# Performance work log

Measured on AMD Instinct MI355X. Metric: run time of the kernel, lower is better.

## Reference

```python
import jax, jax.numpy as jnp
import numpy as np

NEG_SLOPE = 0.2  # DenseGATConv default negative_slope


def dense_gat(x, adj, W, att_src, att_dst, bias):
    # x: [B,N,Cin], adj: [B,N,N] (self-loops already added), W: [Cin,H*C]
    B, N, _ = x.shape
    H, C = att_src.shape
    h = (x @ W).reshape(B, N, H, C)
    a_src = jnp.einsum('bnhc,hc->bnh', h, att_src)  # [B,N,H]
    a_dst = jnp.einsum('bnhc,hc->bnh', h, att_dst)
    # alpha[b,i,j,h] = a_src[b,j,h] + a_dst[b,i,h]  (softmax over j, axis=2)
    alpha = a_src[:, None, :, :] + a_dst[:, :, None, :]
    alpha = jnp.where(alpha >= 0, alpha, NEG_SLOPE * alpha)  # leaky_relu
    mask = (adj != 0)[..., None]  # [B,N,N,1]
    alpha = jax.nn.softmax(jnp.where(mask, alpha, -1e30), axis=2)
    out = jnp.einsum('bijh,bjhc->bihc', alpha, h).reshape(B, N, H * C)
    return out + bias


def setup_inputs() -> dict:
    key = jax.random.key(0)
    ks = jax.random.split(key, 8)
    B, N, D = 1, 8192, 128
    x = jax.random.normal(ks[0], (B, N, D), dtype=jnp.float32)
    adj = (jax.random.uniform(ks[1], (B, N, N)) < 0.01).astype(jnp.float32)
    idx = jnp.arange(N)
    adj = adj.at[:, idx, idx].set(1.0)  # DenseGATConv add_loop=True
    s = 1.0 / np.sqrt(D)
    lin = lambda k: jax.random.uniform(k, (D, D), minval=-s, maxval=s, dtype=jnp.float32)
    att = lambda k: jax.random.normal(k, (1, D), dtype=jnp.float32) * 0.1  # heads=1
    return dict(
        x=x, adj=adj,
        W0=lin(ks[2]), att_src0=att(ks[3]), att_dst0=att(ks[4]), b0=jnp.zeros((D,), jnp.float32),
        W1=lin(ks[5]), att_src1=att(ks[6]), att_dst1=att(ks[7]), b1=jnp.zeros((D,), jnp.float32),
    )


def reference(x, adj, W0, att_src0, att_dst0, b0, W1, att_src1, att_dst1, b1):
    out0 = dense_gat(x, adj, W0, att_src0, att_dst0, b0)
    out0 = jax.nn.relu(out0)  # relu_layers_index = [0]
    out1 = dense_gat(out0, adj, W1, att_src1, att_dst1, b1)
    # dropout_rate = 0 -> dropout is identity; squeeze batch dim as in block
    return (out0[0], out1[0])
```

## Files before the change

### kernel.cpp

```cpp
#include <hip/hip_runtime.h>

#define MAXDEG 192
#define NEG_SLOPE 0.2f
#define D 128

__device__ __forceinline__ float bf2f(unsigned short u) {
    return __uint_as_float(((unsigned)u) << 16);
}
__device__ __forceinline__ unsigned short f2bf(float f) {
    unsigned u = __float_as_uint(f);
    return (unsigned short)((u + 0x7fffu + ((u >> 16) & 1u)) >> 16);
}
__device__ __forceinline__ int is_f32(const void* adj) {
    return ((const unsigned*)adj)[0] == 0x3F800000u;
}

__global__ __launch_bounds__(256) void build_ell(
        const void* __restrict__ adj,
        unsigned short* __restrict__ cols, int* __restrict__ deg, int N) {
    __shared__ int cnt[4];
    const int w = threadIdx.x >> 6, lane = threadIdx.x & 63;
    const int row = blockIdx.x * 4 + w;
    if (lane == 0) cnt[w] = 0;
    __syncthreads();
    unsigned short* crow = cols + (size_t)row * MAXDEG;
    if (is_f32(adj)) {
        const float4* arow = (const float4*)((const float*)adj + (size_t)row * N);
        const int nv = N / 4;
        for (int v = lane; v < nv; v += 128) {
            float4 u0 = arow[v];
            float4 u1 = arow[v + 64];
            const unsigned* a0 = (const unsigned*)&u0;
            const unsigned* a1 = (const unsigned*)&u1;
            #pragma unroll
            for (int e = 0; e < 4; e++)
                if (a0[e]) { int p = atomicAdd(&cnt[w], 1); if (p < MAXDEG) crow[p] = (unsigned short)(v * 4 + e); }
            #pragma unroll
            for (int e = 0; e < 4; e++)
                if (a1[e]) { int p = atomicAdd(&cnt[w], 1); if (p < MAXDEG) crow[p] = (unsigned short)((v + 64) * 4 + e); }
        }
    } else {
        const uint4* arow = (const uint4*)((const unsigned short*)adj + (size_t)row * N);
        const int nv = N / 8;
        for (int v = lane; v < nv; v += 128) {
            uint4 u0 = arow[v];
            uint4 u1 = arow[v + 64];
            const unsigned short* s0 = (const unsigned short*)&u0;
            const unsigned short* s1 = (const unsigned short*)&u1;
            #pragma unroll
            for (int e = 0; e < 8; e++)
                if (s0[e]) { int p = atomicAdd(&cnt[w], 1); if (p < MAXDEG) crow[p] = (unsigned short)(v * 8 + e); }
            #pragma unroll
            for (int e = 0; e < 8; e++)
                if (s1[e]) { int p = atomicAdd(&cnt[w], 1); if (p < MAXDEG) crow[p] = (unsigned short)((v + 64) * 8 + e); }
        }
    }
    __syncthreads();
    if (lane == 0) deg[row] = cnt[w] < MAXDEG ? cnt[w] : MAXDEG;
}

__global__ __launch_bounds__(256) void gemm128(
        const void* __restrict__ A, const void* __restrict__ W,
        const void* __restrict__ adjFlag, float* __restrict__ H,
        const void* __restrict__ attS, const void* __restrict__ attD,
        float* __restrict__ asrc, float* __restrict__ adst, int a_force_f32) {
    __shared__ float xs[32 * D];
    __shared__ float wsf[64 * D];
    const int tid = threadIdx.x;
    const size_t row0 = (size_t)blockIdx.x * 32;
    const int f32m = is_f32(adjFlag);
    const int aF = a_force_f32 | f32m;

    if (aF) {
        const float4* av = (const float4*)((const float*)A + row0 * D);
        float4* xl = (float4*)xs;
        #pragma unroll
        for (int k = 0; k < 4; k++) xl[tid + 256 * k] = av[tid + 256 * k];
    } else {
        const uint4* av = (const uint4*)((const unsigned short*)A + row0 * D);
        #pragma unroll
        for (int k = 0; k < 2; k++) {
            uint4 u = av[tid + 256 * k];
            const unsigned short* us = (const unsigned short*)&u;
            #pragma unroll
            for (int e = 0; e < 8; e++) xs[(tid + 256 * k) * 8 + e] = bf2f(us[e]);
        }
    }

    const int tx = tid & 31, ty = tid >> 5;
    const int c0 = tx * 4, r0 = ty * 4;
    float acc[4][4] = {};
    for (int p = 0; p < 2; p++) {
        __syncthreads();
        if (f32m) {
            const float4* wv = (const float4*)((const float*)W + (size_t)p * 64 * D);
            float4* wl = (float4*)wsf;
            #pragma unroll
            for (int k = 0; k < 8; k++) wl[tid + 256 * k] = wv[tid + 256 * k];
        } else {
            const uint4* wv = (const uint4*)((const unsigned short*)W + (size_t)p * 64 * D);
            #pragma unroll
            for (int k = 0; k < 4; k++) {
                uint4 u = wv[tid + 256 * k];
                const unsigned short* us = (const unsigned short*)&u;
                #pragma unroll
                for (int e = 0; e < 8; e++) wsf[(tid + 256 * k) * 8 + e] = bf2f(us[e]);
            }
        }
        __syncthreads();
        #pragma unroll 8
        for (int k = 0; k < 64; k++) {
            float4 wv = *(const float4*)&wsf[k * D + c0];
            #pragma unroll
            for (int i = 0; i < 4; i++) {
                float xv = xs[(r0 + i) * D + p * 64 + k];
                acc[i][0] += xv * wv.x; acc[i][1] += xv * wv.y;
                acc[i][2] += xv * wv.z; acc[i][3] += xv * wv.w;
            }
        }
    }
    float* Ho = H + row0 * D;
    #pragma unroll
    for (int i = 0; i < 4; i++)
        *(float4*)&Ho[(r0 + i) * D + c0] =
            make_float4(acc[i][0], acc[i][1], acc[i][2], acc[i][3]);

    float aSv[4], aDv[4];
    #pragma unroll
    for (int j = 0; j < 4; j++) {
        aSv[j] = f32m ? ((const float*)attS)[c0 + j] : bf2f(((const unsigned short*)attS)[c0 + j]);
        aDv[j] = f32m ? ((const float*)attD)[c0 + j] : bf2f(((const unsigned short*)attD)[c0 + j]);
    }
    #pragma unroll
    for (int i = 0; i < 4; i++) {
        float s = acc[i][0] * aSv[0] + acc[i][1] * aSv[1] + acc[i][2] * aSv[2] + acc[i][3] * aSv[3];
        float d = acc[i][0] * aDv[0] + acc[i][1] * aDv[1] + acc[i][2] * aDv[2] + acc[i][3] * aDv[3];
        #pragma unroll
        for (int off = 16; off > 0; off >>= 1) {
            s += __shfl_down(s, off, 32);
            d += __shfl_down(d, off, 32);
        }
        if (tx == 0) {
            asrc[row0 + r0 + i] = s;
            adst[row0 + r0 + i] = d;
        }
    }
}

__global__ __launch_bounds__(256) void aggregate(
        const float* __restrict__ H,
        const float* __restrict__ asrc, const float* __restrict__ adst,
        const unsigned short* __restrict__ cols, const int* __restrict__ deg,
        const void* __restrict__ bias, const void* __restrict__ adjFlag,
        float* __restrict__ outF, void* __restrict__ outAny,
        size_t elemOff, int relu) {
    __shared__ float scn[4][MAXDEG];
    __shared__ unsigned short sjj[4][MAXDEG];
    const int w = threadIdx.x >> 6, lane = threadIdx.x & 63;
    const int i = blockIdx.x * 4 + w;
    const int d = deg[i];
    const float ai = adst[i];
    const unsigned short* crow = cols + (size_t)i * MAXDEG;

    const int s0 = lane, s1 = lane + 64, s2 = lane + 128;
    unsigned short j0 = 0, j1 = 0, j2 = 0;
    float e0 = -3e38f, e1 = -3e38f, e2 = -3e38f;
    if (s0 < d) { j0 = crow[s0]; float e = asrc[j0] + ai; e0 = (e >= 0.f) ? e : NEG_SLOPE * e; }
    if (s1 < d) { j1 = crow[s1]; float e = asrc[j1] + ai; e1 = (e >= 0.f) ? e : NEG_SLOPE * e; }
    if (s2 < d) { j2 = crow[s2]; float e = asrc[j2] + ai; e2 = (e >= 0.f) ? e : NEG_SLOPE * e; }
    float m = fmaxf(e0, fmaxf(e1, e2));
    #pragma unroll
    for (int off = 1; off < 64; off <<= 1) m = fmaxf(m, __shfl_xor(m, off));
    float p0 = (s0 < d) ? __expf(e0 - m) : 0.f;
    float p1 = (s1 < d) ? __expf(e1 - m) : 0.f;
    float p2 = (s2 < d) ? __expf(e2 - m) : 0.f;
    float l = p0 + p1 + p2;
    #pragma unroll
    for (int off = 1; off < 64; off <<= 1) l += __shfl_xor(l, off);
    const float invl = 1.f / l;
    scn[w][s0] = p0 * invl; sjj[w][s0] = j0;
    scn[w][s1] = p1 * invl; sjj[w][s1] = j1;
    scn[w][s2] = p2 * invl; sjj[w][s2] = j2;
    __syncthreads();

    const float2* H2 = (const float2*)H;
    float2 a0 = {0.f, 0.f}, a1 = {0.f, 0.f}, a2 = {0.f, 0.f}, a3 = {0.f, 0.f};
    int k = 0;
    for (; k + 3 < d; k += 4) {
        const int ja = sjj[w][k], jb = sjj[w][k + 1], jc = sjj[w][k + 2], jd = sjj[w][k + 3];
        const float wa = scn[w][k], wb = scn[w][k + 1], wc = scn[w][k + 2], wd = scn[w][k + 3];
        const float2 va = H2[(size_t)ja * 64 + lane];
        const float2 vb = H2[(size_t)jb * 64 + lane];
        const float2 vc = H2[(size_t)jc * 64 + lane];
        const float2 vd = H2[(size_t)jd * 64 + lane];
        a0.x += wa * va.x; a0.y += wa * va.y;
        a1.x += wb * vb.x; a1.y += wb * vb.y;
        a2.x += wc * vc.x; a2.y += wc * vc.y;
        a3.x += wd * vd.x; a3.y += wd * vd.y;
    }
    for (; k < d; k++) {
        const int j = sjj[w][k];
        const float wk = scn[w][k];
        const float2 v = H2[(size_t)j * 64 + lane];
        a0.x += wk * v.x; a0.y += wk * v.y;
    }
    float vx = a0.x + a1.x + a2.x + a3.x;
    float vy = a0.y + a1.y + a2.y + a3.y;

    const int f32m = is_f32(adjFlag);
    const int c0 = lane * 2;
    const float b0 = f32m ? ((const float*)bias)[c0]     : bf2f(((const unsigned short*)bias)[c0]);
    const float b1 = f32m ? ((const float*)bias)[c0 + 1] : bf2f(((const unsigned short*)bias)[c0 + 1]);
    vx += b0; vy += b1;
    if (relu) { vx = fmaxf(vx, 0.f); vy = fmaxf(vy, 0.f); }
    if (outF) ((float2*)outF)[(size_t)i * 64 + lane] = make_float2(vx, vy);
    if (f32m) {
        ((float2*)outAny)[(elemOff >> 1) + (size_t)i * 64 + lane] = make_float2(vx, vy);
    } else {
        unsigned packed = (unsigned)f2bf(vx) | ((unsigned)f2bf(vy) << 16);
        ((unsigned*)outAny)[(elemOff >> 1) + (size_t)i * 64 + lane] = packed;
    }
}

extern "C" void kernel_launch(void* const* d_in, const int* in_sizes, int n_in,
                              void* d_out, int out_size, void* d_ws, size_t ws_size,
                              hipStream_t stream) {
    const int N = in_sizes[0] / D;

    char* w = (char*)d_ws;
    int* deg             = (int*)w;            w += (size_t)N * sizeof(int);
    unsigned short* cols = (unsigned short*)w; w += (size_t)N * MAXDEG * sizeof(unsigned short);
    float* h             = (float*)w;          w += (size_t)N * D * sizeof(float);
    float* out0          = (float*)w;          w += (size_t)N * D * sizeof(float);
    float* asrc          = (float*)w;          w += (size_t)N * sizeof(float);
    float* adst          = (float*)w;

    const void* adj = d_in[1];

    build_ell<<<N / 4, 256, 0, stream>>>(adj, cols, deg, N);

    gemm128<<<N / 32, 256, 0, stream>>>(d_in[0], d_in[2], adj, h,
                                        d_in[3], d_in[4], asrc, adst, 0);
    aggregate<<<N / 4, 256, 0, stream>>>(h, asrc, adst, cols, deg, d_in[5], adj,
                                         out0, d_out, 0, 1);

    gemm128<<<N / 32, 256, 0, stream>>>(out0, d_in[6], adj, h,
                                        d_in[7], d_in[8], asrc, adst, 1);
    aggregate<<<N / 4, 256, 0, stream>>>(h, asrc, adst, cols, deg, d_in[9], adj,
                                         nullptr, d_out, (size_t)N * D, 0);
}
```

Measured before the change: 459.0 us.

## Fuse all GAT stages into one persistent kernel with grid barriers

Replaces the five kernel launches with a single persistent kernel of 1024 blocks that runs layer-0 GEMM, ELL construction, aggregation, layer-1 GEMM and aggregation in sequence, separated by atomic-counter grid barriers. ELL rows are handed out dynamically through an atomic work queue so that GEMM blocks overlap with adjacency scanning. The GEMM weight staging is cut to 32-row chunks so shared memory fits four blocks per CU. The aim is to remove launch gaps and tail effects, at the cost of barrier spin overhead and a deadlock risk if not all 1024 blocks are co-resident.

```diff
diff --git a/kernel.cpp b/kernel.cpp
--- a/kernel.cpp
+++ b/kernel.cpp
@@ -3,6 +3,8 @@
 #define MAXDEG 192
 #define NEG_SLOPE 0.2f
 #define D 128
+#define NBLK 1024
+#define TPB 256
 
 __device__ __forceinline__ float bf2f(unsigned short u) {
     return __uint_as_float(((unsigned)u) << 16);
@@ -15,16 +17,29 @@
     return ((const unsigned*)adj)[0] == 0x3F800000u;
 }
 
-__global__ __launch_bounds__(256) void build_ell(
-        const void* __restrict__ adj,
-        unsigned short* __restrict__ cols, int* __restrict__ deg, int N) {
-    __shared__ int cnt[4];
+__device__ __forceinline__ void grid_sync(int* bar, int target) {
+    __syncthreads();
+    __threadfence();
+    if (threadIdx.x == 0) {
+        atomicAdd(bar, 1);
+        while (__hip_atomic_load(bar, __ATOMIC_RELAXED, __HIP_MEMORY_SCOPE_AGENT) < target)
+            __builtin_amdgcn_s_sleep(2);
+    }
+    __syncthreads();
+    __threadfence();
+}
+
+__device__ __forceinline__ void ell_group(
+        int g, const void* __restrict__ adj, int N, int f32m,
+        unsigned short* __restrict__ cols, int* __restrict__ deg,
+        float* __restrict__ smem) {
+    int* cnt = (int*)smem;
     const int w = threadIdx.x >> 6, lane = threadIdx.x & 63;
-    const int row = blockIdx.x * 4 + w;
+    const int row = g * 4 + w;
     if (lane == 0) cnt[w] = 0;
     __syncthreads();
     unsigned short* crow = cols + (size_t)row * MAXDEG;
-    if (is_f32(adj)) {
+    if (f32m) {
         const float4* arow = (const float4*)((const float*)adj + (size_t)row * N);
         const int nv = N / 4;
         for (int v = lane; v < nv; v += 128) {
@@ -59,17 +74,15 @@
     if (lane == 0) deg[row] = cnt[w] < MAXDEG ? cnt[w] : MAXDEG;
 }
 
-__global__ __launch_bounds__(256) void gemm128(
-        const void* __restrict__ A, const void* __restrict__ W,
-        const void* __restrict__ adjFlag, float* __restrict__ H,
-        const void* __restrict__ attS, const void* __restrict__ attD,
-        float* __restrict__ asrc, float* __restrict__ adst, int a_force_f32) {
-    __shared__ float xs[32 * D];
-    __shared__ float wsf[64 * D];
+__device__ __forceinline__ void gemm_tile(
+        int t, const void* __restrict__ A, const void* __restrict__ W,
+        int aF, int f32m, const void* __restrict__ attS, const void* __restrict__ attD,
+        float* __restrict__ H, float* __restrict__ asrc, float* __restrict__ adst,
+        float* __restrict__ smem) {
+    float* xs = smem;
+    float* ws = smem + 4096;
     const int tid = threadIdx.x;
-    const size_t row0 = (size_t)blockIdx.x * 32;
-    const int f32m = is_f32(adjFlag);
-    const int aF = a_force_f32 | f32m;
+    const size_t row0 = (size_t)t * 32;
 
     if (aF) {
         const float4* av = (const float4*)((const float*)A + row0 * D);
@@ -90,30 +103,30 @@
     const int tx = tid & 31, ty = tid >> 5;
     const int c0 = tx * 4, r0 = ty * 4;
     float acc[4][4] = {};
-    for (int p = 0; p < 2; p++) {
+    for (int p = 0; p < 4; p++) {
         __syncthreads();
         if (f32m) {
-            const float4* wv = (const float4*)((const float*)W + (size_t)p * 64 * D);
-            float4* wl = (float4*)wsf;
-            #pragma unroll
-            for (int k = 0; k < 8; k++) wl[tid + 256 * k] = wv[tid + 256 * k];
+            const float4* wv = (const float4*)((const float*)W + (size_t)p * 32 * D);
+            float4* wl = (float4*)ws;
+            #pragma unroll
+            for (int k = 0; k < 4; k++) wl[tid + 256 * k] = wv[tid + 256 * k];
         } else {
-            const uint4* wv = (const uint4*)((const unsigned short*)W + (size_t)p * 64 * D);
-            #pragma unroll
-            for (int k = 0; k < 4; k++) {
+            const uint4* wv = (const uint4*)((const unsigned short*)W + (size_t)p * 32 * D);
+            #pragma unroll
+            for (int k = 0; k < 2; k++) {
                 uint4 u = wv[tid + 256 * k];
                 const unsigned short* us = (const unsigned short*)&u;
                 #pragma unroll
-                for (int e = 0; e < 8; e++) wsf[(tid + 256 * k) * 8 + e] = bf2f(us[e]);
+                for (int e = 0; e < 8; e++) ws[(tid + 256 * k) * 8 + e] = bf2f(us[e]);
             }
         }
         __syncthreads();
         #pragma unroll 8
-        for (int k = 0; k < 64; k++) {
-            float4 wv = *(const float4*)&wsf[k * D + c0];
+        for (int k = 0; k < 32; k++) {
+            float4 wv = *(const float4*)&ws[k * D + c0];
             #pragma unroll
             for (int i = 0; i < 4; i++) {
-                float xv = xs[(r0 + i) * D + p * 64 + k];
+                float xv = xs[(r0 + i) * D + p * 32 + k];
                 acc[i][0] += xv * wv.x; acc[i][1] += xv * wv.y;
                 acc[i][2] += xv * wv.z; acc[i][3] += xv * wv.w;
             }
@@ -147,20 +160,19 @@
     }
 }
 
-__global__ __launch_bounds__(256) void aggregate(
-        const float* __restrict__ H,
+__device__ __forceinline__ void agg_row(
+        int row, const float* __restrict__ H,
         const float* __restrict__ asrc, const float* __restrict__ adst,
         const unsigned short* __restrict__ cols, const int* __restrict__ deg,
-        const void* __restrict__ bias, const void* __restrict__ adjFlag,
+        const void* __restrict__ bias, int f32m,
         float* __restrict__ outF, void* __restrict__ outAny,
-        size_t elemOff, int relu) {
-    __shared__ float scn[4][MAXDEG];
-    __shared__ unsigned short sjj[4][MAXDEG];
+        size_t off2, int relu, float* __restrict__ smem) {
     const int w = threadIdx.x >> 6, lane = threadIdx.x & 63;
-    const int i = blockIdx.x * 4 + w;
-    const int d = deg[i];
-    const float ai = adst[i];
-    const unsigned short* crow = cols + (size_t)i * MAXDEG;
+    float* scn = smem + w * MAXDEG;
+    unsigned short* sjj = (unsigned short*)(smem + 4 * MAXDEG) + w * MAXDEG;
+    const int d = deg[row];
+    const float ai = adst[row];
+    const unsigned short* crow = cols + (size_t)row * MAXDEG;
 
     const int s0 = lane, s1 = lane + 64, s2 = lane + 128;
     unsigned short j0 = 0, j1 = 0, j2 = 0;
@@ -178,17 +190,16 @@
     #pragma unroll
     for (int off = 1; off < 64; off <<= 1) l += __shfl_xor(l, off);
     const float invl = 1.f / l;
-    scn[w][s0] = p0 * invl; sjj[w][s0] = j0;
-    scn[w][s1] = p1 * invl; sjj[w][s1] = j1;
-    scn[w][s2] = p2 * invl; sjj[w][s2] = j2;
-    __syncthreads();
+    scn[s0] = p0 * invl; sjj[s0] = j0;
+    scn[s1] = p1 * invl; sjj[s1] = j1;
+    scn[s2] = p2 * invl; sjj[s2] = j2;
 
     const float2* H2 = (const float2*)H;
-    float2 a0 = {0.f, 0.f}, a1 = {0.f, 0.f}, a2 = {0.f, 0.f}, a3 = {0.f, 0.f};
+    float2 a0 = make_float2(0.f, 0.f), a1 = a0, a2 = a0, a3 = a0;
     int k = 0;
     for (; k + 3 < d; k += 4) {
-        const int ja = sjj[w][k], jb = sjj[w][k + 1], jc = sjj[w][k + 2], jd = sjj[w][k + 3];
-        const float wa = scn[w][k], wb = scn[w][k + 1], wc = scn[w][k + 2], wd = scn[w][k + 3];
+        const int ja = sjj[k], jb = sjj[k + 1], jc = sjj[k + 2], jd = sjj[k + 3];
+        const float wa = scn[k], wb = scn[k + 1], wc = scn[k + 2], wd = scn[k + 3];
         const float2 va = H2[(size_t)ja * 64 + lane];
         const float2 vb = H2[(size_t)jb * 64 + lane];
         const float2 vc = H2[(size_t)jc * 64 + lane];
@@ -199,26 +210,75 @@
         a3.x += wd * vd.x; a3.y += wd * vd.y;
     }
     for (; k < d; k++) {
-        const int j = sjj[w][k];
-        const float wk = scn[w][k];
+        const int j = sjj[k];
+        const float wk = scn[k];
         const float2 v = H2[(size_t)j * 64 + lane];
         a0.x += wk * v.x; a0.y += wk * v.y;
     }
     float vx = a0.x + a1.x + a2.x + a3.x;
     float vy = a0.y + a1.y + a2.y + a3.y;
 
-    const int f32m = is_f32(adjFlag);
     const int c0 = lane * 2;
-    const float b0 = f32m ? ((const float*)bias)[c0]     : bf2f(((const unsigned short*)bias)[c0]);
-    const float b1 = f32m ? ((const float*)bias)[c0 + 1] : bf2f(((const unsigned short*)bias)[c0 + 1]);
-    vx += b0; vy += b1;
+    const float bx = f32m ? ((const float*)bias)[c0]     : bf2f(((const unsigned short*)bias)[c0]);
+    const float by = f32m ? ((const float*)bias)[c0 + 1] : bf2f(((const unsigned short*)bias)[c0 + 1]);
+    vx += bx; vy += by;
     if (relu) { vx = fmaxf(vx, 0.f); vy = fmaxf(vy, 0.f); }
-    if (outF) ((float2*)outF)[(size_t)i * 64 + lane] = make_float2(vx, vy);
+    if (outF) ((float2*)outF)[(size_t)row * 64 + lane] = make_float2(vx, vy);
     if (f32m) {
-        ((float2*)outAny)[(elemOff >> 1) + (size_t)i * 64 + lane] = make_float2(vx, vy);
+        ((float2*)outAny)[off2 + (size_t)row * 64 + lane] = make_float2(vx, vy);
     } else {
         unsigned packed = (unsigned)f2bf(vx) | ((unsigned)f2bf(vy) << 16);
-        ((unsigned*)outAny)[(elemOff >> 1) + (size_t)i * 64 + lane] = packed;
+        ((unsigned*)outAny)[off2 + (size_t)row * 64 + lane] = packed;
+    }
+}
+
+__global__ __launch_bounds__(TPB, 4) void gat_mega(
+        const void* __restrict__ x, const void* __restrict__ adj,
+        const void* __restrict__ W0, const void* __restrict__ aS0,
+        const void* __restrict__ aD0, const void* __restrict__ b0,
+        const void* __restrict__ W1, const void* __restrict__ aS1,
+        const void* __restrict__ aD1, const void* __restrict__ b1,
+        void* __restrict__ out, int N,
+        int* __restrict__ bar, int* __restrict__ qhead,
+        int* __restrict__ deg, unsigned short* __restrict__ cols,
+        float* __restrict__ h, float* __restrict__ out0,
+        float* __restrict__ asrc, float* __restrict__ adst) {
+    __shared__ float smem[8192];
+    __shared__ int sgrp;
+    const int bid = blockIdx.x, tid = threadIdx.x;
+    const int f32m = is_f32(adj);
+    const int GT = N / 32;
+    const int NG = N / 4;
+
+    if (bid < GT)
+        gemm_tile(bid, x, W0, f32m, f32m, aS0, aD0, h, asrc, adst, smem);
+    __syncthreads();
+    for (;;) {
+        if (tid == 0) sgrp = atomicAdd(qhead, 1);
+        __syncthreads();
+        const int g = sgrp;
+        __syncthreads();
+        if (g >= NG) break;
+        ell_group(g, adj, N, f32m, cols, deg, smem);
+    }
+    grid_sync(bar, NBLK);
+
+    {
+        const int gw = bid * 4 + (tid >> 6);
+        for (int r = gw; r < N; r += NBLK * 4)
+            agg_row(r, h, asrc, adst, cols, deg, b0, f32m, out0, out, 0, 1, smem);
+    }
+    grid_sync(bar, 2 * NBLK);
+
+    if (bid < GT)
+        gemm_tile(bid, out0, W1, 1, f32m, aS1, aD1, h, asrc, adst, smem);
+    grid_sync(bar, 3 * NBLK);
+
+    {
+        const int gw = bid * 4 + (tid >> 6);
+        for (int r = gw; r < N; r += NBLK * 4)
+            agg_row(r, h, asrc, adst, cols, deg, b1, f32m, nullptr, out,
+                    (size_t)N * (D / 2), 0, smem);
     }
 }
 
@@ -228,6 +288,9 @@
     const int N = in_sizes[0] / D;
 
     char* w = (char*)d_ws;
+    int* bar             = (int*)w;
+    int* qhead           = (int*)(w + 64);
+    w += 256;
     int* deg             = (int*)w;            w += (size_t)N * sizeof(int);
     unsigned short* cols = (unsigned short*)w; w += (size_t)N * MAXDEG * sizeof(unsigned short);
     float* h             = (float*)w;          w += (size_t)N * D * sizeof(float);
@@ -235,17 +298,10 @@
     float* asrc          = (float*)w;          w += (size_t)N * sizeof(float);
     float* adst          = (float*)w;
 
-    const void* adj = d_in[1];
-
-    build_ell<<<N / 4, 256, 0, stream>>>(adj, cols, deg, N);
-
-    gemm128<<<N / 32, 256, 0, stream>>>(d_in[0], d_in[2], adj, h,
-                                        d_in[3], d_in[4], asrc, adst, 0);
-    aggregate<<<N / 4, 256, 0, stream>>>(h, asrc, adst, cols, deg, d_in[5], adj,
-                                         out0, d_out, 0, 1);
-
-    gemm128<<<N / 32, 256, 0, stream>>>(out0, d_in[6], adj, h,
-                                        d_in[7], d_in[8], asrc, adst, 1);
-    aggregate<<<N / 4, 256, 0, stream>>>(h, asrc, adst, cols, deg, d_in[9], adj,
-                                         nullptr, d_out, (size_t)N * D, 0);
-}
+    hipMemsetAsync(d_ws, 0, 256, stream);
+
+    gat_mega<<<NBLK, TPB, 0, stream>>>(
+        d_in[0], d_in[1], d_in[2], d_in[3], d_in[4], d_in[5],
+        d_in[6], d_in[7], d_in[8], d_in[9],
+        d_out, N, bar, qhead, deg, cols, h, out0, asrc, adst);
+}
```

Result: slower. 1.150 ms (+150.5%).
